# Kernel tuning notes

Hardware: AMD Instinct MI355X
Metric: run time of the kernel (lower is better)

The kernel has to match this reference:

```python
import jax, jax.numpy as jnp
import numpy as np
from jax import lax

DIM = 96
HEADS = 4
HID = int(DIM * 2.66)  # 255
EPS_LN = 1e-5
EPS_NORM = 1e-12


def _ln(x, w, b):
    # channel-wise LayerNorm over c of (b,c,h,w) (equivalent to to_3d -> LN(c) -> to_4d)
    mu = x.mean(axis=1, keepdims=True)
    var = ((x - mu) ** 2).mean(axis=1, keepdims=True)
    return (x - mu) / jnp.sqrt(var + EPS_LN) * w[None, :, None, None] + b[None, :, None, None]


def _c1x1(w, x):
    # 1x1 conv, no bias: w (out,in), x (b,in,h,w)
    return jnp.einsum('oc,bchw->bohw', w, x)


def _l2norm(x):
    # F.normalize along last dim (pixels), eps=1e-12
    n = jnp.sqrt(jnp.sum(x * x, axis=-1, keepdims=True))
    return x / jnp.maximum(n, EPS_NORM)


def setup_inputs() -> dict:
    key = jax.random.key(0)
    ks = jax.random.split(key, 10)
    B, H, W = 4, 256, 256
    s = 0.02
    return {
        'x': jax.random.normal(ks[0], (B, DIM, H, W), jnp.float32),
        'svp_fea': jax.random.normal(ks[1], (B, 3, H, W), jnp.float32),
        'norm1_w': jnp.ones((DIM,), jnp.float32),
        'norm1_b': jnp.zeros((DIM,), jnp.float32),
        'qkv_w': jax.random.normal(ks[2], (3 * DIM, DIM), jnp.float32) * s,
        'qkv_dw_w': jax.random.normal(ks[3], (3 * DIM, 1, 3, 3), jnp.float32) * s,
        'svp_w': jax.random.normal(ks[4], (3 * HEADS, 3), jnp.float32) * s,
        'temperature': jnp.ones((HEADS, 1, 1), jnp.float32),
        'proj_out_w': jax.random.normal(ks[5], (DIM, DIM + 3 * HEADS), jnp.float32) * s,
        'norm2_w': jnp.ones((DIM,), jnp.float32),
        'norm2_b': jnp.zeros((DIM,), jnp.float32),
        'ffn1_w': jax.random.normal(ks[6], (HID, DIM), jnp.float32) * s,
        'ffn2_w': jax.random.normal(ks[7], (HID, DIM), jnp.float32) * s,
        'ffn_out_w': jax.random.normal(ks[8], (DIM, HID), jnp.float32) * s,
    }


def reference(x, svp_fea, norm1_w, norm1_b, qkv_w, qkv_dw_w, svp_w, temperature,
              proj_out_w, norm2_w, norm2_b, ffn1_w, ffn2_w, ffn_out_w):
    b, c, h, w = x.shape
    hw = h * w
    # --- IlluminationGuideAttention ---
    xn = _ln(x, norm1_w, norm1_b)
    qkv = _c1x1(qkv_w, xn)
    qkv = lax.conv_general_dilated(
        qkv, qkv_dw_w, window_strides=(1, 1), padding='SAME',
        feature_group_count=3 * DIM, dimension_numbers=('NCHW', 'OIHW', 'NCHW'))
    q, k, v = jnp.split(qkv, 3, axis=1)
    svp_q = _c1x1(svp_w, svp_fea)

    def heads(t):
        return t.reshape(b, HEADS, -1, hw)  # b head c (h w)

    q = _l2norm(heads(q))          # (b,H,ch,hw)
    k = _l2norm(heads(k))
    svp_q = _l2norm(heads(svp_q))  # (b,H,3,hw)
    v = heads(v)
    q = jnp.concatenate([q, svp_q], axis=2)  # (b,H,ch+3,hw)

    attn = jnp.einsum('bhcn,bhdn->bhcd', q, k) * temperature[None]
    attn = jax.nn.softmax(attn, axis=-1)
    out = jnp.einsum('bhcd,bhdn->bhcn', attn, v).reshape(b, -1, h, w)
    x = x + _c1x1(proj_out_w, out)

    # --- DualGatedFeedForward ---
    xn = _ln(x, norm2_w, norm2_b)
    p1 = _c1x1(ffn1_w, xn)
    p2 = _c1x1(ffn2_w, xn)
    g = p1 * jax.nn.sigmoid(p2) + p2 * jax.nn.gelu(p1, approximate=False)
    return x + _c1x1(ffn_out_w, g)
```

## Files before the change

### kernel.cpp

```cpp
#include <hip/hip_runtime.h>


namespace {
constexpr int kB = 4;
constexpr int kC = 96;
constexpr int kHW = 65536;
constexpr int kNP = kB * kHW;
constexpr int kQKVC = 288;
constexpr int kNH = 4;
constexpr int kCH = 24;
constexpr int kQC = 27;
constexpr int kHID = 255;
constexpr int kSTR = 40;
constexpr int kBST = 104;
constexpr int kQKSPLIT = 32;
}

typedef __attribute__((ext_vector_type(8))) short short8;
typedef __attribute__((ext_vector_type(8))) unsigned short ushort8;
typedef __attribute__((ext_vector_type(4))) unsigned short ushortx4;
typedef __attribute__((ext_vector_type(4))) float floatx4;

__device__ __forceinline__ float bf2f(unsigned short u) {
  return __uint_as_float(((unsigned int)u) << 16);
}
__device__ __forceinline__ unsigned short f2bf(float f) {
  unsigned int i = __float_as_uint(f);
  i += 0x7fffu + ((i >> 16) & 1u);
  return (unsigned short)(i >> 16);
}

__global__ void k_zero(float* __restrict__ p, int n) {
  const int i = blockIdx.x * blockDim.x + threadIdx.x;
  if (i < n) p[i] = 0.f;
}
__global__ void k_fill0_f32(float* __restrict__ p, int n) {
  const int i = blockIdx.x * blockDim.x + threadIdx.x;
  if (i < n) p[i] = 0.f;
}

__global__ __launch_bounds__(256) void k_wconv(
    const float* __restrict__ qkvw, const float* __restrict__ projw,
    const float* __restrict__ w1, const float* __restrict__ w2,
    const float* __restrict__ fw, unsigned short* __restrict__ qb,
    unsigned short* __restrict__ pb, unsigned short* __restrict__ w1b,
    unsigned short* __restrict__ w2b, unsigned short* __restrict__ fwb) {
  int i = blockIdx.x * 256 + threadIdx.x;
  if (i < 27648) { qb[i] = f2bf(qkvw[i]); return; }
  i -= 27648;
  if (i < 12288) {
    const int r = i >> 7, k = i & 127;
    pb[i] = (k < 108) ? f2bf(projw[r * 108 + k]) : (unsigned short)0;
    return;
  }
  i -= 12288;
  if (i < 24576) { w1b[i] = (i < 24480) ? f2bf(w1[i]) : (unsigned short)0; return; }
  i -= 24576;
  if (i < 24576) { w2b[i] = (i < 24480) ? f2bf(w2[i]) : (unsigned short)0; return; }
  i -= 24576;
  {
    const int r = i >> 8, k = i & 255;
    fwb[i] = (k < 255) ? f2bf(fw[r * 255 + k]) : (unsigned short)0;
  }
}

__global__ __launch_bounds__(256) void k_ln1_apply(
    const float* __restrict__ x, const float* __restrict__ nw,
    const float* __restrict__ nb, unsigned short* __restrict__ A) {
  const int pg = blockIdx.x * 256 + threadIdx.x;
  const int b = pg >> 16, p = pg & (kHW - 1);
  const float* xb = x + (size_t)b * kC * kHW + p;
  float v[kC];
  float s = 0.f, s2 = 0.f;
  #pragma unroll
  for (int c = 0; c < kC; ++c) {
    v[c] = xb[(size_t)c * kHW];
    s += v[c];
    s2 = fmaf(v[c], v[c], s2);
  }
  const float m = s * (1.f / kC);
  const float var = s2 * (1.f / kC) - m * m;
  const float rstd = rsqrtf(var + 1e-5f);
  unsigned short* ob = A + ((size_t)b * kQKVC + 192) * kHW + p;
  #pragma unroll
  for (int c = 0; c < kC; ++c) {
    ob[(size_t)c * kHW] = f2bf((v[c] - m) * rstd * nw[c] + nb[c]);
  }
}

__global__ __launch_bounds__(256) void k_gemm_qkv(
    const unsigned short* __restrict__ xn1base, const unsigned short* __restrict__ qb,
    int grp, unsigned short* __restrict__ bufC) {
  __shared__ __align__(16) unsigned short As[96 * kSTR];
  __shared__ __align__(16) unsigned short Bs[128 * kSTR];
  const int tid = threadIdx.x;
  const int b = blockIdx.y;
  const int p0 = blockIdx.x * 128;
  const int wave = tid >> 6, lane = tid & 63, ln16 = lane & 15, quad = lane >> 4;
  floatx4 acc[6][2];
  #pragma unroll
  for (int i = 0; i < 6; ++i) { acc[i][0] = (floatx4)(0.f); acc[i][1] = (floatx4)(0.f); }
  const int rB = tid >> 3, c0 = (tid & 7) * 16;
  const int pos = rB ^ ((tid & 3) << 3);
  const int q0 = (quad ^ ((wave * 2) & 3)) << 3;
  const int q1 = (quad ^ ((wave * 2 + 1) & 3)) << 3;
  for (int ks = 0; ks < 3; ++ks) {
    const int k0 = ks * 32;
    for (int idx = tid; idx < 384; idx += 256) {
      const int m = idx >> 2, ch = idx & 3;
      *(short8*)&As[m * kSTR + ch * 8] =
          *(const short8*)(qb + (size_t)(grp * 96 + m) * 96 + k0 + ch * 8);
    }
    {
      const unsigned short* src =
          xn1base + ((size_t)b * kQKVC + 192 + k0 + rB) * kHW + p0 + c0;
      const ushort8 u0 = ((const ushort8*)src)[0];
      const ushort8 u1 = ((const ushort8*)src)[1];
      #pragma unroll
      for (int e = 0; e < 8; ++e) {
        Bs[(c0 + e) * kSTR + pos] = u0[e];
        Bs[(c0 + 8 + e) * kSTR + pos] = u1[e];
      }
    }
    __syncthreads();
    short8 bfr0 = *(const short8*)&Bs[(wave * 32 + ln16) * kSTR + q0];
    short8 bfr1 = *(const short8*)&Bs[(wave * 32 + 16 + ln16) * kSTR + q1];
    #pragma unroll
    for (int ms = 0; ms < 6; ++ms) {
      const short8 afr = *(const short8*)&As[(ms * 16 + ln16) * kSTR + quad * 8];
      acc[ms][0] = __builtin_amdgcn_mfma_f32_16x16x32_bf16(afr, bfr0, acc[ms][0], 0, 0, 0);
      acc[ms][1] = __builtin_amdgcn_mfma_f32_16x16x32_bf16(afr, bfr1, acc[ms][1], 0, 0, 0);
    }
    __syncthreads();
  }
  unsigned short* ob = bufC + (size_t)b * kC * kHW;
  #pragma unroll
  for (int ms = 0; ms < 6; ++ms)
    #pragma unroll
    for (int ns = 0; ns < 2; ++ns)
      #pragma unroll
      for (int r = 0; r < 4; ++r) {
        const int R = ms * 16 + quad * 4 + r;
        const int P = p0 + wave * 32 + ns * 16 + ln16;
        ob[(size_t)R * kHW + P] = f2bf(acc[ms][ns][r]);
      }
}

__global__ __launch_bounds__(256) void k_gemm_proj(
    const unsigned short* __restrict__ qkv_post, const unsigned short* __restrict__ pb,
    const float* __restrict__ x, unsigned short* __restrict__ x2,
    float* __restrict__ mu2, float* __restrict__ rs2) {
  __shared__ __align__(16) unsigned short As[96 * kSTR];
  __shared__ __align__(16) unsigned short Bs[128 * kSTR];
  const int tid = threadIdx.x;
  const int b = blockIdx.y;
  const int p0 = blockIdx.x * 128;
  const int wave = tid >> 6, lane = tid & 63, ln16 = lane & 15, quad = lane >> 4;
  floatx4 acc[6][2];
  #pragma unroll
  for (int i = 0; i < 6; ++i) { acc[i][0] = (floatx4)(0.f); acc[i][1] = (floatx4)(0.f); }
  const int rB = tid >> 3, c0 = (tid & 7) * 16;
  const int pos = rB ^ ((tid & 3) << 3);
  const int q0 = (quad ^ ((wave * 2) & 3)) << 3;
  const int q1 = (quad ^ ((wave * 2 + 1) & 3)) << 3;
  for (int ks = 0; ks < 4; ++ks) {
    const int k0 = ks * 32;
    for (int idx = tid; idx < 384; idx += 256) {
      const int m = idx >> 2, ch = idx & 3;
      *(short8*)&As[m * kSTR + ch * 8] =
          *(const short8*)(pb + (size_t)m * 128 + k0 + ch * 8);
    }
    {
      const int k = k0 + rB;
      if (k < 108) {
        const unsigned short* src = qkv_post + ((size_t)b * kQKVC + k) * kHW + p0 + c0;
        const ushort8 u0 = ((const ushort8*)src)[0];
        const ushort8 u1 = ((const ushort8*)src)[1];
        #pragma unroll
        for (int e = 0; e < 8; ++e) {
          Bs[(c0 + e) * kSTR + pos] = u0[e];
          Bs[(c0 + 8 + e) * kSTR + pos] = u1[e];
        }
      } else {
        #pragma unroll
        for (int e = 0; e < 16; ++e) Bs[(c0 + e) * kSTR + pos] = 0;
      }
    }
    __syncthreads();
    short8 bfr0 = *(const short8*)&Bs[(wave * 32 + ln16) * kSTR + q0];
    short8 bfr1 = *(const short8*)&Bs[(wave * 32 + 16 + ln16) * kSTR + q1];
    #pragma unroll
    for (int ms = 0; ms < 6; ++ms) {
      const short8 afr = *(const short8*)&As[(ms * 16 + ln16) * kSTR + quad * 8];
      acc[ms][0] = __builtin_amdgcn_mfma_f32_16x16x32_bf16(afr, bfr0, acc[ms][0], 0, 0, 0);
      acc[ms][1] = __builtin_amdgcn_mfma_f32_16x16x32_bf16(afr, bfr1, acc[ms][1], 0, 0, 0);
    }
    __syncthreads();
  }
  float s[2] = {0.f, 0.f}, s2[2] = {0.f, 0.f};
  #pragma unroll
  for (int ms = 0; ms < 6; ++ms)
    #pragma unroll
    for (int ns = 0; ns < 2; ++ns)
      #pragma unroll
      for (int r = 0; r < 4; ++r) {
        const int R = ms * 16 + quad * 4 + r;
        const int P = p0 + wave * 32 + ns * 16 + ln16;
        const size_t idx = ((size_t)b * kC + R) * kHW + P;
        const float val = acc[ms][ns][r] + x[idx];
        x2[idx] = f2bf(val);
        s[ns] += val;
        s2[ns] = fmaf(val, val, s2[ns]);
      }
  #pragma unroll
  for (int ns = 0; ns < 2; ++ns) {
    float a = s[ns], c = s2[ns];
    a += __shfl_xor(a, 16); a += __shfl_xor(a, 32);
    c += __shfl_xor(c, 16); c += __shfl_xor(c, 32);
    if (quad == 0) {
      const int P = p0 + wave * 32 + ns * 16 + ln16;
      const float m = a * (1.f / kC);
      mu2[(b << 16) + P] = m;
      rs2[(b << 16) + P] = rsqrtf(c * (1.f / kC) - m * m + 1e-5f);
    }
  }
}

__global__ __launch_bounds__(256) void k_gemm_gatefout(
    const unsigned short* __restrict__ x2, const float* __restrict__ mu_buf,
    const float* __restrict__ rs_buf, const float* __restrict__ nw,
    const float* __restrict__ nb, const unsigned short* __restrict__ w1b,
    const unsigned short* __restrict__ w2b, const unsigned short* __restrict__ fwb,
    float* __restrict__ out) {
  __shared__ __align__(16) unsigned short Bs[128 * kBST];
  __shared__ __align__(16) unsigned short As[128 * kSTR];
  __shared__ __align__(16) unsigned int Gs[128 * 32];
  __shared__ float mus[128], rss[128];
  const int tid = threadIdx.x;
  const int b = blockIdx.y;
  const int p0 = blockIdx.x * 128;
  if (tid < 128) {
    mus[tid] = mu_buf[(b << 16) + p0 + tid];
    rss[tid] = rs_buf[(b << 16) + p0 + tid];
  }
  __syncthreads();
  const int wave = tid >> 6, lane = tid & 63, ln16 = lane & 15, quad = lane >> 4;
  const int rB = tid >> 3, c0 = (tid & 7) * 16;
  const int pos = rB ^ ((tid & 3) << 3);
  const int q0 = (quad ^ ((wave * 2) & 3)) << 3;
  const int q1 = (quad ^ ((wave * 2 + 1) & 3)) << 3;
  const int l7 = ln16 & 7;
  #pragma unroll
  for (int ks = 0; ks < 3; ++ks) {
    const int k = ks * 32 + rB;
    const float wk = nw[k], bk = nb[k];
    const unsigned short* src = x2 + ((size_t)b * kC + k) * kHW + p0 + c0;
    const ushort8 u0 = ((const ushort8*)src)[0];
    const ushort8 u1 = ((const ushort8*)src)[1];
    #pragma unroll
    for (int e = 0; e < 8; ++e) {
      const int n0 = c0 + e, n1 = c0 + 8 + e;
      Bs[n0 * kBST + ks * 32 + pos] = f2bf((bf2f(u0[e]) - mus[n0]) * rss[n0] * wk + bk);
      Bs[n1 * kBST + ks * 32 + pos] = f2bf((bf2f(u1[e]) - mus[n1]) * rss[n1] * wk + bk);
    }
  }
  floatx4 facc[6][2];
  #pragma unroll
  for (int i = 0; i < 6; ++i) { facc[i][0] = (floatx4)(0.f); facc[i][1] = (floatx4)(0.f); }
  for (int grp = 0; grp < 4; ++grp) {
    const int i0 = grp * 64;
    floatx4 acc[8][2];
    #pragma unroll
    for (int i = 0; i < 8; ++i) { acc[i][0] = (floatx4)(0.f); acc[i][1] = (floatx4)(0.f); }
    #pragma unroll
    for (int ks = 0; ks < 3; ++ks) {
      for (int idx = tid; idx < 512; idx += 256) {
        const int m = idx >> 2, ch = idx & 3;
        const int ii = i0 + (m & 63);
        const unsigned short* wsrc =
            ((m < 64) ? w1b : w2b) + (size_t)ii * 96 + ks * 32 + ch * 8;
        *(short8*)&As[m * kSTR + ch * 8] = *(const short8*)wsrc;
      }
      __syncthreads();
      short8 bfr0 = *(const short8*)&Bs[(wave * 32 + ln16) * kBST + ks * 32 + q0];
      short8 bfr1 = *(const short8*)&Bs[(wave * 32 + 16 + ln16) * kBST + ks * 32 + q1];
      #pragma unroll
      for (int ms = 0; ms < 8; ++ms) {
        const short8 afr = *(const short8*)&As[(ms * 16 + ln16) * kSTR + quad * 8];
        acc[ms][0] = __builtin_amdgcn_mfma_f32_16x16x32_bf16(afr, bfr0, acc[ms][0], 0, 0, 0);
        acc[ms][1] = __builtin_amdgcn_mfma_f32_16x16x32_bf16(afr, bfr1, acc[ms][1], 0, 0, 0);
      }
      __syncthreads();
    }
    #pragma unroll
    for (int ms = 0; ms < 4; ++ms)
      #pragma unroll
      for (int ns = 0; ns < 2; ++ns) {
        const int pl = wave * 32 + ns * 16 + ln16;
        #pragma unroll
        for (int rr = 0; rr < 2; ++rr) {
          float gv[2];
          #pragma unroll
          for (int h = 0; h < 2; ++h) {
            const float p1 = acc[ms][ns][rr * 2 + h], p2 = acc[ms + 4][ns][rr * 2 + h];
            const float sig = __builtin_amdgcn_rcpf(1.f + __expf(-p2));
            const float targ = p1 * fmaf(p1 * p1, 0.0713548f, 1.5957691f);
            const float gel = p1 * __builtin_amdgcn_rcpf(1.f + __expf(-targ));
            gv[h] = fmaf(p1, sig, p2 * gel);
          }
          const int dj = ms * 8 + quad * 2 + rr;
          const int djs = dj ^ (l7 << 2);
          Gs[pl * 32 + djs] = (unsigned int)f2bf(gv[0]) | ((unsigned int)f2bf(gv[1]) << 16);
        }
      }
    __syncthreads();
    #pragma unroll
    for (int ksub = 0; ksub < 2; ++ksub) {
      for (int idx = tid; idx < 384; idx += 256) {
        const int m = idx >> 2, ch = idx & 3;
        *(short8*)&As[m * kSTR + ch * 8] =
            *(const short8*)(fwb + (size_t)m * 256 + i0 + ksub * 32 + ch * 8);
      }
      __syncthreads();
      const int bka = ((ksub * 4 + quad) ^ l7) * 4;
      const short8 bf0 = *(const short8*)&Gs[(wave * 32 + ln16) * 32 + bka];
      const short8 bf1 = *(const short8*)&Gs[(wave * 32 + 16 + ln16) * 32 + bka];
      #pragma unroll
      for (int ms = 0; ms < 6; ++ms) {
        const short8 afr = *(const short8*)&As[(ms * 16 + ln16) * kSTR + quad * 8];
        facc[ms][0] = __builtin_amdgcn_mfma_f32_16x16x32_bf16(afr, bf0, facc[ms][0], 0, 0, 0);
        facc[ms][1] = __builtin_amdgcn_mfma_f32_16x16x32_bf16(afr, bf1, facc[ms][1], 0, 0, 0);
      }
      __syncthreads();
    }
  }
  #pragma unroll
  for (int ms = 0; ms < 6; ++ms)
    #pragma unroll
    for (int ns = 0; ns < 2; ++ns)
      #pragma unroll
      for (int r = 0; r < 4; ++r) {
        const int R = ms * 16 + quad * 4 + r;
        const int P = p0 + wave * 32 + ns * 16 + ln16;
        const size_t idx = ((size_t)b * kC + R) * kHW + P;
        out[idx] = facc[ms][ns][r] + bf2f(x2[idx]);
      }
}

__global__ __launch_bounds__(256) void k_dw(
    const unsigned short* __restrict__ buf, const float* __restrict__ dww,
    unsigned short* __restrict__ qkv_post, int gbase) {
  const int blk = blockIdx.x;
  const int plane = blk >> 4;
  const int yg = (blk & 15) * 16;
  const int b = plane / kC, chl = plane % kC;
  const int t = threadIdx.x;
  const int y = yg + (t >> 5) * 2;
  const int x0 = (t & 31) * 8;
  const unsigned short* in = buf + (size_t)plane * kHW;
  float w[9];
  #pragma unroll
  for (int i = 0; i < 9; ++i) w[i] = dww[(size_t)(gbase + chl) * 9 + i];
  float acc0[8], acc1[8];
  #pragma unroll
  for (int j = 0; j < 8; ++j) { acc0[j] = 0.f; acc1[j] = 0.f; }
  #pragma unroll
  for (int dy = -1; dy <= 2; ++dy) {
    const int yy = y + dy;
    if (yy < 0 || yy > 255) continue;
    const unsigned short* rp = in + yy * 256;
    float f[10];
    const ushort8 v = *(const ushort8*)(rp + x0);
    #pragma unroll
    for (int e = 0; e < 8; ++e) f[e + 1] = bf2f(v[e]);
    f[0] = (x0 > 0) ? bf2f(rp[x0 - 1]) : 0.f;
    f[9] = (x0 < 248) ? bf2f(rp[x0 + 8]) : 0.f;
    if (dy <= 1) {
      const float w0 = w[(dy + 1) * 3], w1 = w[(dy + 1) * 3 + 1], w2 = w[(dy + 1) * 3 + 2];
      #pragma unroll
      for (int j = 0; j < 8; ++j)
        acc0[j] = fmaf(w0, f[j], fmaf(w1, f[j + 1], fmaf(w2, f[j + 2], acc0[j])));
    }
    if (dy >= 0) {
      const float w0 = w[dy * 3], w1 = w[dy * 3 + 1], w2 = w[dy * 3 + 2];
      #pragma unroll
      for (int j = 0; j < 8; ++j)
        acc1[j] = fmaf(w0, f[j], fmaf(w1, f[j + 1], fmaf(w2, f[j + 2], acc1[j])));
    }
  }
  unsigned short* op = qkv_post + ((size_t)b * kQKVC + gbase + chl) * kHW + y * 256 + x0;
  ushort8 o0, o1;
  #pragma unroll
  for (int j = 0; j < 8; ++j) { o0[j] = f2bf(acc0[j]); o1[j] = f2bf(acc1[j]); }
  *(ushort8*)op = o0;
  *(ushort8*)(op + 256) = o1;
}

__global__ __launch_bounds__(256) void k_svpq(
    const float* __restrict__ svp, const float* __restrict__ svpw,
    unsigned short* __restrict__ svpq) {
  const int t8 = blockIdx.x * 256 + threadIdx.x;
  const int b = t8 >> 13, p0 = (t8 & 8191) * 8;
  float s0[8], s1[8], s2v[8];
  #pragma unroll
  for (int j = 0; j < 8; ++j) {
    s0[j] = svp[((size_t)b * 3 + 0) * kHW + p0 + j];
    s1[j] = svp[((size_t)b * 3 + 1) * kHW + p0 + j];
    s2v[j] = svp[((size_t)b * 3 + 2) * kHW + p0 + j];
  }
  #pragma unroll
  for (int jj = 0; jj < 12; ++jj) {
    const float w0 = svpw[jj * 3], w1 = svpw[jj * 3 + 1], w2 = svpw[jj * 3 + 2];
    ushort8 o;
    #pragma unroll
    for (int j = 0; j < 8; ++j)
      o[j] = f2bf(fmaf(w2, s2v[j], fmaf(w1, s1[j], w0 * s0[j])));
    *(ushort8*)&svpq[((size_t)b * 12 + jj) * kHW + p0] = o;
  }
}

__global__ __launch_bounds__(256) void k_qk(
    const unsigned short* __restrict__ qkv_post, const unsigned short* __restrict__ svpq,
    float* __restrict__ spart, float* __restrict__ ssbuf) {
  const int bh = blockIdx.y, b = bh >> 2, h = bh & 3;
  const int tid = threadIdx.x;
  const int wave = tid >> 6, lane = tid & 63;
  const int l15 = lane & 15, gq = lane >> 4;
  const int pstart = blockIdx.x * 2048 + wave * 512;
  constexpr int NCH = 16;

  const unsigned short* pA0 =
      qkv_post + ((size_t)b * kQKVC + h * kCH + l15) * kHW + gq * 8;
  const unsigned short* pB0 =
      qkv_post + ((size_t)b * kQKVC + 96 + h * kCH + l15) * kHW + gq * 8;
  const int rA1 = 16 + l15, rB1 = 16 + l15;
  const bool vA1 = (rA1 < kQC), vB1 = (rB1 < kCH);
  const unsigned short* pA1 =
      (rA1 < kCH) ? qkv_post + ((size_t)b * kQKVC + h * kCH + rA1) * kHW + gq * 8
      : (rA1 < kQC) ? svpq + ((size_t)(b * 12 + h * 3 + (rA1 - kCH))) * kHW + gq * 8
                    : pA0;
  const unsigned short* pB1 =
      vB1 ? qkv_post + ((size_t)b * kQKVC + 96 + h * kCH + rB1) * kHW + gq * 8 : pB0;

  floatx4 c00 = (floatx4)(0.f), c01 = (floatx4)(0.f);
  floatx4 c10 = (floatx4)(0.f), c11 = (floatx4)(0.f);
  float ssA0 = 0.f, ssA1 = 0.f, ssB0 = 0.f, ssB1 = 0.f;
  const short8 kZ = (short8)(short)0;

  short8 a0 = *(const short8*)(pA0 + pstart);
  short8 b0 = *(const short8*)(pB0 + pstart);
  short8 a1 = vA1 ? *(const short8*)(pA1 + pstart) : kZ;
  short8 b1 = vB1 ? *(const short8*)(pB1 + pstart) : kZ;
  for (int c = 0; c < NCH; ++c) {
    const short8 ta0 = a0, tb0 = b0, ta1 = a1, tb1 = b1;
    if (c + 1 < NCH) {
      const int pn = pstart + (c + 1) * 32;
      a0 = *(const short8*)(pA0 + pn);
      b0 = *(const short8*)(pB0 + pn);
      a1 = vA1 ? *(const short8*)(pA1 + pn) : kZ;
      b1 = vB1 ? *(const short8*)(pB1 + pn) : kZ;
    }
    c00 = __builtin_amdgcn_mfma_f32_16x16x32_bf16(ta0, tb0, c00, 0, 0, 0);
    c01 = __builtin_amdgcn_mfma_f32_16x16x32_bf16(ta0, tb1, c01, 0, 0, 0);
    c10 = __builtin_amdgcn_mfma_f32_16x16x32_bf16(ta1, tb0, c10, 0, 0, 0);
    c11 = __builtin_amdgcn_mfma_f32_16x16x32_bf16(ta1, tb1, c11, 0, 0, 0);
    #pragma unroll
    for (int e = 0; e < 8; ++e) {
      const float v0 = bf2f((unsigned short)ta0[e]);
      const float v1 = bf2f((unsigned short)ta1[e]);
      const float v2 = bf2f((unsigned short)tb0[e]);
      const float v3 = bf2f((unsigned short)tb1[e]);
      ssA0 = fmaf(v0, v0, ssA0);
      ssA1 = fmaf(v1, v1, ssA1);
      ssB0 = fmaf(v2, v2, ssB0);
      ssB1 = fmaf(v3, v3, ssB1);
    }
  }
  ssA0 += __shfl_xor(ssA0, 16); ssA0 += __shfl_xor(ssA0, 32);
  ssA1 += __shfl_xor(ssA1, 16); ssA1 += __shfl_xor(ssA1, 32);
  ssB0 += __shfl_xor(ssB0, 16); ssB0 += __shfl_xor(ssB0, 32);
  ssB1 += __shfl_xor(ssB1, 16); ssB1 += __shfl_xor(ssB1, 32);
  if (gq == 0) {
    atomicAdd(&ssbuf[b * 96 + h * kCH + l15], ssA0);
    if (rA1 < kCH) atomicAdd(&ssbuf[b * 96 + h * kCH + rA1], ssA1);
    else if (rA1 < kQC) atomicAdd(&ssbuf[768 + b * 12 + h * 3 + (rA1 - kCH)], ssA1);
    atomicAdd(&ssbuf[384 + b * 96 + h * kCH + l15], ssB0);
    if (vB1) atomicAdd(&ssbuf[384 + b * 96 + h * kCH + rB1], ssB1);
  }
  float* wp = spart + ((size_t)((blockIdx.x * 16 + bh) * 4 + wave)) * 648;
  #pragma unroll
  for (int r = 0; r < 4; ++r) {
    const int row0 = gq * 4 + r, row1 = 16 + gq * 4 + r;
    wp[row0 * kCH + l15] = c00[r];
    if (16 + l15 < kCH) wp[row0 * kCH + 16 + l15] = c01[r];
    if (row1 < kQC) {
      wp[row1 * kCH + l15] = c10[r];
      if (16 + l15 < kCH) wp[row1 * kCH + 16 + l15] = c11[r];
    }
  }
}

__global__ __launch_bounds__(256) void k_softmax(
    const float* __restrict__ spart, const float* __restrict__ ssbuf,
    const float* __restrict__ temp, float* __restrict__ attn) {
  const int row = blockIdx.x * 256 + threadIdx.x;
  if (row >= kB * kNH * kQC) return;
  const int bh = row / kQC, c = row - bh * kQC;
  const int b = bh >> 2, h = bh & 3;
  const float ssq = (c < kCH) ? ssbuf[b * 96 + h * kCH + c]
                              : ssbuf[768 + b * 12 + h * 3 + (c - kCH)];
  const float rq = 1.f / fmaxf(sqrtf(ssq), 1e-12f);
  const float t = temp[h];
  float l[kCH];
  #pragma unroll
  for (int d = 0; d < kCH; ++d) l[d] = 0.f;
  for (int s = 0; s < kQKSPLIT * 4; ++s) {
    const int split = s >> 2, wv = s & 3;
    const float* sp = spart + ((size_t)((split * 16 + bh) * 4 + wv)) * 648 + c * kCH;
    #pragma unroll
    for (int d = 0; d < kCH; ++d) l[d] += sp[d];
  }
  float mx = -1e30f;
  #pragma unroll
  for (int d = 0; d < kCH; ++d) {
    const float rk = 1.f / fmaxf(sqrtf(ssbuf[384 + b * 96 + h * kCH + d]), 1e-12f);
    l[d] = l[d] * rq * rk * t;
    mx = fmaxf(mx, l[d]);
  }
  float sum = 0.f;
  #pragma unroll
  for (int d = 0; d < kCH; ++d) { l[d] = __expf(l[d] - mx); sum += l[d]; }
  const float inv = 1.f / sum;
  float* arow = attn + (size_t)(bh * kQC + c) * kCH;
  #pragma unroll
  for (int d = 0; d < kCH; ++d) arow[d] = l[d] * inv;
}

__global__ __launch_bounds__(256) void k_av(
    const float* __restrict__ attn, unsigned short* __restrict__ qkv_post) {
  const int h = blockIdx.y;
  const int t4 = blockIdx.x * 256 + threadIdx.x;
  const int b = t4 >> 14, p0 = (t4 & 16383) * 4;
  __shared__ float at[kQC * kCH];
  for (int idx = threadIdx.x; idx < kQC * kCH; idx += 256)
    at[idx] = attn[(size_t)(b * kNH + h) * kQC * kCH + idx];
  __syncthreads();
  float acc[kQC][4];
  #pragma unroll
  for (int c = 0; c < kQC; ++c)
    #pragma unroll
    for (int j = 0; j < 4; ++j) acc[c][j] = 0.f;
  for (int d = 0; d < kCH; ++d) {
    const ushortx4 v =
        *(const ushortx4*)&qkv_post[((size_t)b * kQKVC + 192 + h * kCH + d) * kHW + p0];
    float vv[4];
    #pragma unroll
    for (int j = 0; j < 4; ++j) vv[j] = bf2f(v[j]);
    #pragma unroll
    for (int c = 0; c < kQC; ++c) {
      const float a = at[c * kCH + d];
      #pragma unroll
      for (int j = 0; j < 4; ++j) acc[c][j] = fmaf(a, vv[j], acc[c][j]);
    }
  }
  #pragma unroll
  for (int c = 0; c < kQC; ++c) {
    ushortx4 o;
    #pragma unroll
    for (int j = 0; j < 4; ++j) o[j] = f2bf(acc[c][j]);
    *(ushortx4*)&qkv_post[((size_t)b * kQKVC + h * kQC + c) * kHW + p0] = o;
  }
}

extern "C" void kernel_launch(void* const* d_in, const int* in_sizes, int n_in,
                              void* d_out, int out_size, void* d_ws, size_t ws_size,
                              hipStream_t stream) {
  (void)in_sizes; (void)n_in;
  const float* x     = (const float*)d_in[0];
  const float* svp   = (const float*)d_in[1];
  const float* n1w   = (const float*)d_in[2];
  const float* n1b   = (const float*)d_in[3];
  const float* qkvw  = (const float*)d_in[4];
  const float* dww   = (const float*)d_in[5];
  const float* svpw  = (const float*)d_in[6];
  const float* temp  = (const float*)d_in[7];
  const float* projw = (const float*)d_in[8];
  const float* n2w   = (const float*)d_in[9];
  const float* n2b   = (const float*)d_in[10];
  const float* w1    = (const float*)d_in[11];
  const float* w2    = (const float*)d_in[12];
  const float* fw    = (const float*)d_in[13];
  float* outp = (float*)d_out;

  const size_t SZ_A = (size_t)kB * kQKVC * kHW * 2;
  const size_t SZ_C = (size_t)kB * kC * kHW * 2;
  const size_t NEED = (1u << 20) + SZ_A + SZ_C;

  if (ws_size < NEED) {
    k_fill0_f32<<<(out_size + 255) / 256, 256, 0, stream>>>(outp, out_size);
    return;
  }

  char* ws = (char*)d_ws;
  float* attn  = (float*)(ws + 65536);
  float* ssbuf = (float*)(ws + 131072);
  unsigned short* qb  = (unsigned short*)(ws + 262144);
  unsigned short* pb  = (unsigned short*)(ws + 317440);
  unsigned short* w1b = (unsigned short*)(ws + 342016);
  unsigned short* w2b = (unsigned short*)(ws + 391168);
  unsigned short* fwb = (unsigned short*)(ws + 440320);
  unsigned short* A    = (unsigned short*)(ws + (1u << 20));
  unsigned short* bufC = (unsigned short*)(ws + (1u << 20) + SZ_A);
  float* mu2 = (float*)(ws + (1u << 20) + 134u * 1048576u);
  float* rs2 = (float*)(ws + (1u << 20) + 135u * 1048576u);
  unsigned short* x2   = bufC;
  unsigned short* svpq = bufC;
  float* spart = (float*)(ws + (1u << 20) + SZ_A + 8u * 1048576u);

  k_wconv<<<444, 256, 0, stream>>>(qkvw, projw, w1, w2, fw, qb, pb, w1b, w2b, fwb);
  k_zero<<<4, 256, 0, stream>>>(ssbuf, 816);
  k_ln1_apply<<<kNP / 256, 256, 0, stream>>>(x, n1w, n1b, A);
  for (int grp = 0; grp < 3; ++grp) {
    k_gemm_qkv<<<dim3(kHW / 128, kB), 256, 0, stream>>>(A, qb, grp, bufC);
    k_dw<<<kB * kC * 16, 256, 0, stream>>>(bufC, dww, A, grp * kC);
  }
  k_svpq<<<kNP / 8 / 256, 256, 0, stream>>>(svp, svpw, svpq);
  k_qk<<<dim3(kQKSPLIT, 16), 256, 0, stream>>>(A, svpq, spart, ssbuf);
  k_softmax<<<2, 256, 0, stream>>>(spart, ssbuf, temp, attn);
  k_av<<<dim3(kNP / 4 / 256, kNH), 256, 0, stream>>>(attn, A);
  k_gemm_proj<<<dim3(kHW / 128, kB), 256, 0, stream>>>(A, pb, x, x2, mu2, rs2);
  k_gemm_gatefout<<<dim3(kHW / 128, kB), 256, 0, stream>>>(
      x2, mu2, rs2, n2w, n2b, w1b, w2b, fwb, outp);
}
```

Measured before the change: 639.2 us.

## Fuse three QKV GEMM passes into one kernel reusing LN1 tile, use packed bf16 converts

The three per-group QKV GEMM launches become one kernel that loads the normalized input tile into shared memory once and computes all 288 output channels. Results go to scratch slots, including A regions already consumed, so the three depthwise convs can run afterwards in an order that avoids overwriting live data. Separately, software bf16 rounding is replaced by the hardware v_cvt_pk_bf16_f32 packed conversion across all kernels. Together these cut repeated input reads, launch count and conversion ALU work, in exchange for more shared memory per block and a delicate buffer-aliasing order.

```diff
diff --git a/kernel.cpp b/kernel.cpp
--- a/kernel.cpp
+++ b/kernel.cpp
@@ -20,6 +20,8 @@
 typedef __attribute__((ext_vector_type(8))) unsigned short ushort8;
 typedef __attribute__((ext_vector_type(4))) unsigned short ushortx4;
 typedef __attribute__((ext_vector_type(4))) float floatx4;
+typedef __attribute__((ext_vector_type(4))) unsigned int uintx4;
+typedef __attribute__((ext_vector_type(2))) unsigned int uintx2;
 
 __device__ __forceinline__ float bf2f(unsigned short u) {
   return __uint_as_float(((unsigned int)u) << 16);
@@ -28,6 +30,14 @@
   unsigned int i = __float_as_uint(f);
   i += 0x7fffu + ((i >> 16) & 1u);
   return (unsigned short)(i >> 16);
+}
+__device__ __forceinline__ unsigned int pk2_bf16(float lo, float hi) {
+  unsigned int r;
+  asm("v_cvt_pk_bf16_f32 %0, %1, %2" : "=v"(r) : "v"(lo), "v"(hi));
+  return r;
+}
+__device__ __forceinline__ unsigned short f2bf_fast(float f) {
+  return (unsigned short)pk2_bf16(f, f);
 }
 
 __global__ void k_zero(float* __restrict__ p, int n) {
@@ -84,66 +94,70 @@
   unsigned short* ob = A + ((size_t)b * kQKVC + 192) * kHW + p;
   #pragma unroll
   for (int c = 0; c < kC; ++c) {
-    ob[(size_t)c * kHW] = f2bf((v[c] - m) * rstd * nw[c] + nb[c]);
-  }
-}
-
-__global__ __launch_bounds__(256) void k_gemm_qkv(
-    const unsigned short* __restrict__ xn1base, const unsigned short* __restrict__ qb,
-    int grp, unsigned short* __restrict__ bufC) {
+    ob[(size_t)c * kHW] = f2bf_fast((v[c] - m) * rstd * nw[c] + nb[c]);
+  }
+}
+
+__global__ __launch_bounds__(256) void k_gemm_qkv3(
+    unsigned short* __restrict__ Abuf, const unsigned short* __restrict__ qb,
+    unsigned short* __restrict__ bufC) {
+  __shared__ __align__(16) unsigned short Bs[128 * kBST];
   __shared__ __align__(16) unsigned short As[96 * kSTR];
-  __shared__ __align__(16) unsigned short Bs[128 * kSTR];
   const int tid = threadIdx.x;
   const int b = blockIdx.y;
   const int p0 = blockIdx.x * 128;
   const int wave = tid >> 6, lane = tid & 63, ln16 = lane & 15, quad = lane >> 4;
-  floatx4 acc[6][2];
-  #pragma unroll
-  for (int i = 0; i < 6; ++i) { acc[i][0] = (floatx4)(0.f); acc[i][1] = (floatx4)(0.f); }
   const int rB = tid >> 3, c0 = (tid & 7) * 16;
   const int pos = rB ^ ((tid & 3) << 3);
   const int q0 = (quad ^ ((wave * 2) & 3)) << 3;
   const int q1 = (quad ^ ((wave * 2 + 1) & 3)) << 3;
+  #pragma unroll
   for (int ks = 0; ks < 3; ++ks) {
-    const int k0 = ks * 32;
-    for (int idx = tid; idx < 384; idx += 256) {
-      const int m = idx >> 2, ch = idx & 3;
-      *(short8*)&As[m * kSTR + ch * 8] =
-          *(const short8*)(qb + (size_t)(grp * 96 + m) * 96 + k0 + ch * 8);
-    }
-    {
-      const unsigned short* src =
-          xn1base + ((size_t)b * kQKVC + 192 + k0 + rB) * kHW + p0 + c0;
-      const ushort8 u0 = ((const ushort8*)src)[0];
-      const ushort8 u1 = ((const ushort8*)src)[1];
-      #pragma unroll
-      for (int e = 0; e < 8; ++e) {
-        Bs[(c0 + e) * kSTR + pos] = u0[e];
-        Bs[(c0 + 8 + e) * kSTR + pos] = u1[e];
-      }
-    }
-    __syncthreads();
-    short8 bfr0 = *(const short8*)&Bs[(wave * 32 + ln16) * kSTR + q0];
-    short8 bfr1 = *(const short8*)&Bs[(wave * 32 + 16 + ln16) * kSTR + q1];
-    #pragma unroll
-    for (int ms = 0; ms < 6; ++ms) {
-      const short8 afr = *(const short8*)&As[(ms * 16 + ln16) * kSTR + quad * 8];
-      acc[ms][0] = __builtin_amdgcn_mfma_f32_16x16x32_bf16(afr, bfr0, acc[ms][0], 0, 0, 0);
-      acc[ms][1] = __builtin_amdgcn_mfma_f32_16x16x32_bf16(afr, bfr1, acc[ms][1], 0, 0, 0);
-    }
-    __syncthreads();
-  }
-  unsigned short* ob = bufC + (size_t)b * kC * kHW;
-  #pragma unroll
-  for (int ms = 0; ms < 6; ++ms)
-    #pragma unroll
-    for (int ns = 0; ns < 2; ++ns)
-      #pragma unroll
-      for (int r = 0; r < 4; ++r) {
-        const int R = ms * 16 + quad * 4 + r;
-        const int P = p0 + wave * 32 + ns * 16 + ln16;
-        ob[(size_t)R * kHW + P] = f2bf(acc[ms][ns][r]);
-      }
+    const unsigned short* src =
+        Abuf + ((size_t)b * kQKVC + 192 + ks * 32 + rB) * kHW + p0 + c0;
+    const ushort8 u0 = ((const ushort8*)src)[0];
+    const ushort8 u1 = ((const ushort8*)src)[1];
+    #pragma unroll
+    for (int e = 0; e < 8; ++e) {
+      Bs[(c0 + e) * kBST + ks * 32 + pos] = u0[e];
+      Bs[(c0 + 8 + e) * kBST + ks * 32 + pos] = u1[e];
+    }
+  }
+  for (int grp = 0; grp < 3; ++grp) {
+    floatx4 acc[6][2];
+    #pragma unroll
+    for (int i = 0; i < 6; ++i) { acc[i][0] = (floatx4)(0.f); acc[i][1] = (floatx4)(0.f); }
+    for (int ks = 0; ks < 3; ++ks) {
+      for (int idx = tid; idx < 384; idx += 256) {
+        const int m = idx >> 2, ch = idx & 3;
+        *(short8*)&As[m * kSTR + ch * 8] =
+            *(const short8*)(qb + (size_t)(grp * 96 + m) * 96 + ks * 32 + ch * 8);
+      }
+      __syncthreads();
+      short8 bfr0 = *(const short8*)&Bs[(wave * 32 + ln16) * kBST + ks * 32 + q0];
+      short8 bfr1 = *(const short8*)&Bs[(wave * 32 + 16 + ln16) * kBST + ks * 32 + q1];
+      #pragma unroll
+      for (int ms = 0; ms < 6; ++ms) {
+        const short8 afr = *(const short8*)&As[(ms * 16 + ln16) * kSTR + quad * 8];
+        acc[ms][0] = __builtin_amdgcn_mfma_f32_16x16x32_bf16(afr, bfr0, acc[ms][0], 0, 0, 0);
+        acc[ms][1] = __builtin_amdgcn_mfma_f32_16x16x32_bf16(afr, bfr1, acc[ms][1], 0, 0, 0);
+      }
+      __syncthreads();
+    }
+    unsigned short* ob = (grp == 0)
+        ? bufC + (size_t)b * kC * kHW
+        : Abuf + ((size_t)b * kQKVC + (grp == 1 ? 0 : 96)) * kHW;
+    #pragma unroll
+    for (int ms = 0; ms < 6; ++ms)
+      #pragma unroll
+      for (int ns = 0; ns < 2; ++ns)
+        #pragma unroll
+        for (int r = 0; r < 4; ++r) {
+          const int R = ms * 16 + quad * 4 + r;
+          const int P = p0 + wave * 32 + ns * 16 + ln16;
+          ob[(size_t)R * kHW + P] = f2bf_fast(acc[ms][ns][r]);
+        }
+  }
 }
 
 __global__ __launch_bounds__(256) void k_gemm_proj(
@@ -208,7 +222,7 @@
         const int P = p0 + wave * 32 + ns * 16 + ln16;
         const size_t idx = ((size_t)b * kC + R) * kHW + P;
         const float val = acc[ms][ns][r] + x[idx];
-        x2[idx] = f2bf(val);
+        x2[idx] = f2bf_fast(val);
         s[ns] += val;
         s2[ns] = fmaf(val, val, s2[ns]);
       }
@@ -260,8 +274,10 @@
     #pragma unroll
     for (int e = 0; e < 8; ++e) {
       const int n0 = c0 + e, n1 = c0 + 8 + e;
-      Bs[n0 * kBST + ks * 32 + pos] = f2bf((bf2f(u0[e]) - mus[n0]) * rss[n0] * wk + bk);
-      Bs[n1 * kBST + ks * 32 + pos] = f2bf((bf2f(u1[e]) - mus[n1]) * rss[n1] * wk + bk);
+      Bs[n0 * kBST + ks * 32 + pos] =
+          f2bf_fast((bf2f(u0[e]) - mus[n0]) * rss[n0] * wk + bk);
+      Bs[n1 * kBST + ks * 32 + pos] =
+          f2bf_fast((bf2f(u1[e]) - mus[n1]) * rss[n1] * wk + bk);
     }
   }
   floatx4 facc[6][2];
@@ -310,7 +326,7 @@
           }
           const int dj = ms * 8 + quad * 2 + rr;
           const int djs = dj ^ (l7 << 2);
-          Gs[pl * 32 + djs] = (unsigned int)f2bf(gv[0]) | ((unsigned int)f2bf(gv[1]) << 16);
+          Gs[pl * 32 + djs] = pk2_bf16(gv[0], gv[1]);
         }
       }
     __syncthreads();
@@ -348,8 +364,8 @@
 }
 
 __global__ __launch_bounds__(256) void k_dw(
-    const unsigned short* __restrict__ buf, const float* __restrict__ dww,
-    unsigned short* __restrict__ qkv_post, int gbase) {
+    const unsigned short* __restrict__ buf, int bstride, int sbase,
+    const float* __restrict__ dww, unsigned short* __restrict__ qkv_post, int gbase) {
   const int blk = blockIdx.x;
   const int plane = blk >> 4;
   const int yg = (blk & 15) * 16;
@@ -357,7 +373,7 @@
   const int t = threadIdx.x;
   const int y = yg + (t >> 5) * 2;
   const int x0 = (t & 31) * 8;
-  const unsigned short* in = buf + (size_t)plane * kHW;
+  const unsigned short* in = buf + ((size_t)(b * bstride + sbase + chl)) * kHW;
   float w[9];
   #pragma unroll
   for (int i = 0; i < 9; ++i) w[i] = dww[(size_t)(gbase + chl) * 9 + i];
@@ -389,11 +405,14 @@
     }
   }
   unsigned short* op = qkv_post + ((size_t)b * kQKVC + gbase + chl) * kHW + y * 256 + x0;
-  ushort8 o0, o1;
-  #pragma unroll
-  for (int j = 0; j < 8; ++j) { o0[j] = f2bf(acc0[j]); o1[j] = f2bf(acc1[j]); }
-  *(ushort8*)op = o0;
-  *(ushort8*)(op + 256) = o1;
+  uintx4 o0, o1;
+  #pragma unroll
+  for (int j = 0; j < 4; ++j) {
+    o0[j] = pk2_bf16(acc0[j * 2], acc0[j * 2 + 1]);
+    o1[j] = pk2_bf16(acc1[j * 2], acc1[j * 2 + 1]);
+  }
+  *(uintx4*)op = o0;
+  *(uintx4*)(op + 256) = o1;
 }
 
 __global__ __launch_bounds__(256) void k_svpq(
@@ -411,11 +430,14 @@
   #pragma unroll
   for (int jj = 0; jj < 12; ++jj) {
     const float w0 = svpw[jj * 3], w1 = svpw[jj * 3 + 1], w2 = svpw[jj * 3 + 2];
-    ushort8 o;
-    #pragma unroll
-    for (int j = 0; j < 8; ++j)
-      o[j] = f2bf(fmaf(w2, s2v[j], fmaf(w1, s1[j], w0 * s0[j])));
-    *(ushort8*)&svpq[((size_t)b * 12 + jj) * kHW + p0] = o;
+    uintx4 o;
+    #pragma unroll
+    for (int j = 0; j < 4; ++j) {
+      const float a = fmaf(w2, s2v[j * 2], fmaf(w1, s1[j * 2], w0 * s0[j * 2]));
+      const float c = fmaf(w2, s2v[j * 2 + 1], fmaf(w1, s1[j * 2 + 1], w0 * s0[j * 2 + 1]));
+      o[j] = pk2_bf16(a, c);
+    }
+    *(uintx4*)&svpq[((size_t)b * 12 + jj) * kHW + p0] = o;
   }
 }
 
@@ -565,10 +587,10 @@
   }
   #pragma unroll
   for (int c = 0; c < kQC; ++c) {
-    ushortx4 o;
-    #pragma unroll
-    for (int j = 0; j < 4; ++j) o[j] = f2bf(acc[c][j]);
-    *(ushortx4*)&qkv_post[((size_t)b * kQKVC + h * kQC + c) * kHW + p0] = o;
+    uintx2 o;
+    o[0] = pk2_bf16(acc[c][0], acc[c][1]);
+    o[1] = pk2_bf16(acc[c][2], acc[c][3]);
+    *(uintx2*)&qkv_post[((size_t)b * kQKVC + h * kQC + c) * kHW + p0] = o;
   }
 }
 
@@ -620,10 +642,10 @@
   k_wconv<<<444, 256, 0, stream>>>(qkvw, projw, w1, w2, fw, qb, pb, w1b, w2b, fwb);
   k_zero<<<4, 256, 0, stream>>>(ssbuf, 816);
   k_ln1_apply<<<kNP / 256, 256, 0, stream>>>(x, n1w, n1b, A);
-  for (int grp = 0; grp < 3; ++grp) {
-    k_gemm_qkv<<<dim3(kHW / 128, kB), 256, 0, stream>>>(A, qb, grp, bufC);
-    k_dw<<<kB * kC * 16, 256, 0, stream>>>(bufC, dww, A, grp * kC);
-  }
+  k_gemm_qkv3<<<dim3(kHW / 128, kB), 256, 0, stream>>>(A, qb, bufC);
+  k_dw<<<kB * kC * 16, 256, 0, stream>>>(A, kQKVC, 96, dww, A, 192);
+  k_dw<<<kB * kC * 16, 256, 0, stream>>>(A, kQKVC, 0, dww, A, 96);
+  k_dw<<<kB * kC * 16, 256, 0, stream>>>(bufC, kC, 0, dww, A, 0);
   k_svpq<<<kNP / 8 / 256, 256, 0, stream>>>(svp, svpw, svpq);
   k_qk<<<dim3(kQKSPLIT, 16), 256, 0, stream>>>(A, svpq, spart, ssbuf);
   k_softmax<<<2, 256, 0, stream>>>(spart, ssbuf, temp, attn);
```

Result: faster. 618.8 us (-3.2%).
